# Optimization experiments

Measured on AMD Instinct MI355X. Metric: run time of the kernel, lower is better.

## Reference

```python
import jax, jax.numpy as jnp
import numpy as np

N = 20000   # nodes
E = 320000  # edges
G = 64      # graphs in batch
IN = 256    # in_dim
H = 256     # hidden_dim1
C = 2       # n_classes


def setup_inputs() -> dict:
    key = jax.random.key(0)
    ks = jax.random.split(key, 12)
    h = jax.random.normal(ks[0], (N, IN), jnp.float32)
    src = jax.random.randint(ks[1], (E,), 0, N)
    dst = jax.random.randint(ks[2], (E,), 0, N)
    graph_id = jnp.sort(jax.random.randint(ks[3], (N,), 0, G))
    s_in = 1.0 / np.sqrt(IN)
    s_h = 1.0 / np.sqrt(H)
    W_conv = jax.random.normal(ks[4], (IN, H), jnp.float32) * s_in
    b_conv = jnp.zeros((H,), jnp.float32)
    w_gate = jax.random.normal(ks[5], (H, 1), jnp.float32) * s_h
    b_gate = jnp.zeros((1,), jnp.float32)
    W1 = jax.random.normal(ks[6], (H, H), jnp.float32) * s_h
    b1 = jnp.zeros((H,), jnp.float32)
    W2 = jax.random.normal(ks[7], (H, C), jnp.float32) * s_h
    b2 = jnp.zeros((C,), jnp.float32)
    return dict(h=h, src=src, dst=dst, graph_id=graph_id, W_conv=W_conv,
                b_conv=b_conv, w_gate=w_gate, b_gate=b_gate, W1=W1, b1=b1,
                W2=W2, b2=b2)


def reference(h, src, dst, graph_id, W_conv, b_conv, w_gate, b_gate, W1, b1, W2, b2):
    ones_e = jnp.ones((E,), jnp.float32)
    # DGL GraphConv, norm='both': D_out^-1/2 on source, D_in^-1/2 on dest
    deg_out = jax.ops.segment_sum(ones_e, src, num_segments=N)
    deg_in = jax.ops.segment_sum(ones_e, dst, num_segments=N)
    hn = h * jax.lax.rsqrt(jnp.maximum(deg_out, 1.0))[:, None]
    hn = hn @ W_conv                       # [N, H] (weight applied before aggregation)
    agg = jax.ops.segment_sum(hn[src], dst, num_segments=N)  # gather + scatter-add
    agg = agg * jax.lax.rsqrt(jnp.maximum(deg_in, 1.0))[:, None] + b_conv
    hr = jax.nn.relu(agg)                  # F.relu after conv1
    # GlobalAttentionPooling: per-graph segment softmax over gate scores
    gate = hr @ w_gate + b_gate            # [N, 1]
    gmax = jax.ops.segment_max(gate, graph_id, num_segments=G)
    e = jnp.exp(gate - gmax[graph_id])
    denom = jax.ops.segment_sum(e, graph_id, num_segments=G)
    att = e / denom[graph_id]              # [N, 1] attention weights (g2)
    hg = jax.ops.segment_sum(att * hr, graph_id, num_segments=G)  # [G, H]
    # classifier heads (dropout is identity at inference)
    a2 = hg @ W1 + b1
    a3 = a2 @ W2 + b2
    return jax.nn.sigmoid(a3), att, hg
```

## Files before the change

### kernel.cpp

```cpp
#include <hip/hip_runtime.h>
#include <hip/hip_bf16.h>
#include <hip/hip_fp16.h>
#include <math.h>

#define NN 20000
#define EE 320000
#define GG 64
#define IND 256
#define HD 256
#define CC 2

typedef __hip_bfloat16 bf16;
typedef __attribute__((ext_vector_type(8))) short short8;
typedef __attribute__((ext_vector_type(4))) float f32x4;

__device__ __forceinline__ float b2f(bf16 x){ return __bfloat162float(x); }
__device__ __forceinline__ float bits2f(unsigned short b){
    union{ float f; unsigned u; } v; v.u = ((unsigned)b) << 16; return v.f;
}
__device__ __forceinline__ short f2bs(float x){
    union{ bf16 b; short s; } u; u.b = __float2bfloat16(x); return u.s;
}
__device__ __forceinline__ float ldf3(const void* p, size_t i, int c){
    if (c == 1) return b2f(((const bf16*)p)[i]);
    if (c == 2) return __half2float(((const __half*)p)[i]);
    return ((const float*)p)[i];
}
__device__ __forceinline__ int idec(const void* p, int i, int c){
    if (c == 1) return (int)(((const long long*)p)[i]);
    if (c == 2) return (int)(((const float*)p)[i]);
    if (c == 3) return (int)__half2float(((const __half*)p)[i]);
    return ((const int*)p)[i];
}
__device__ __forceinline__ int wdetect(const unsigned short* p){
    int cb = 0, cf = 0, nz = 0;
    for (int i = 0; i < 128; i += 2){
        unsigned u = p[i];
        nz += (u != 0);
        int e8 = (u >> 7) & 0xFF;
        int e5 = (u >> 10) & 0x1F;
        cb += (e8 >= 100 && e8 <= 141);
        cf += (e5 >= 4 && e5 <= 22);
    }
    return (nz < 8) ? 0 : (cb >= 60) ? 1 : ((cf >= 60) ? 2 : 0);
}

#define ZBLK 64
__global__ __launch_bounds__(256) void k_detect(const void* src, const void* dst,
                         const void* gid,
                         const unsigned short* h, const unsigned short* Wc,
                         const unsigned short* wg, const unsigned short* W1,
                         const unsigned short* W2, const unsigned short* bc,
                         int* icode, int* dcode, int* zero_base,
                         bf16* __restrict__ Wb){
    int blk = blockIdx.x;
    if (blk < 3){
        if (threadIdx.x != 0) return;
        const void* buf = (blk == 0) ? src : (blk == 1) ? dst : gid;
        int n     = (blk == 2) ? NN : EE;
        int bound = (blk == 2) ? GG : NN;
        int ok64 = 1, ok32 = 1, okf32 = 1, okf16 = 1;
        const long long* p64 = (const long long*)buf;
        for (int i = 0; i < 64; i++){
            long long v = p64[n/8 + i];
            if (v < 0 || v >= (long long)bound) ok64 = 0;
        }
        const int* p32 = (const int*)buf;
        const unsigned* pu = (const unsigned*)buf;
        for (int i = 0; i < 64; i++){
            int v = p32[n/4 + i];
            if (v < 0 || v >= bound) ok32 = 0;
            float f = __uint_as_float(pu[n/4 + i]);
            if (!(f >= 0.f && f < (float)bound)) okf32 = 0;
        }
        const __half* ph = (const __half*)buf;
        for (int i = 0; i < 64; i++){
            float f = __half2float(ph[n/2 + i]);
            if (!(f >= 0.f && f < (float)bound)) okf16 = 0;
        }
        icode[blk] = ok64 ? 1 : (ok32 ? 0 : (okf32 ? 2 : (okf16 ? 3 : 0)));
    } else if (blk == 3){
        int t = threadIdx.x; if (t >= 6) return;
        const unsigned short* p = t==0?h:t==1?Wc:t==2?wg:t==3?W1:t==4?W2:bc;
        dcode[t] = wdetect(p);
    } else if (blk < 4 + IND){
        int k = blk - 4;
        __shared__ int code;
        if (threadIdx.x == 0) code = wdetect(Wc);
        __syncthreads();
        int c = code;
        int n = threadIdx.x;
        Wb[(size_t)n*IND + k] = __float2bfloat16(ldf3(Wc, (size_t)k*HD + n, c));
    } else {
        int idx = (blk - (4 + IND))*256 + threadIdx.x;
        const int total = 3*NN + GG*HD;
        for (int i = idx; i < total; i += ZBLK*256) zero_base[i] = 0;
    }
}

__global__ void k_prep(const void* src_r, const void* dst_r, const void* gid_r,
                       const int* __restrict__ icode,
                       int* __restrict__ gid_i,
                       int* cnt_out, int* cnt_in){
    int i = blockIdx.x*256 + threadIdx.x;
    if (i < NN) gid_i[i] = idec(gid_r, i, icode[2]);
    if (i >= EE) return;
    int s = idec(src_r, i, icode[0]);
    int d = idec(dst_r, i, icode[1]);
    if ((unsigned)s < NN) atomicAdd(&cnt_out[s], 1);
    if ((unsigned)d < NN) atomicAdd(&cnt_in[d], 1);
}

__global__ __launch_bounds__(1024) void k_scan(const int* __restrict__ cnt_out,
                                               const int* __restrict__ cnt_in,
                                               const int* __restrict__ gid,
                                               float* rs_out, float* rs_in,
                                               int* __restrict__ row_start,
                                               int* gstart, int* gend){
    int t = threadIdx.x;
    for (int i = t; i < NN; i += 1024){
        rs_out[i] = rsqrtf(fmaxf((float)cnt_out[i], 1.f));
        rs_in[i]  = rsqrtf(fmaxf((float)cnt_in[i], 1.f));
    }
    __shared__ int part[1024];
    const int per = (NN + 1023)/1024;
    int lo = t*per, hi = min(lo+per, NN);
    int s = 0;
    for (int i = lo; i < hi; i++) s += cnt_in[i];
    part[t] = s; __syncthreads();
    for (int off = 1; off < 1024; off <<= 1){
        int v = (t >= off) ? part[t-off] : 0;
        __syncthreads();
        part[t] += v;
        __syncthreads();
    }
    int base = part[t] - s;
    for (int i = lo; i < hi; i++){ row_start[i] = base; base += cnt_in[i]; }
    if (t == 1023) row_start[NN] = part[1023];
    __shared__ int ls[GG+1];
    if (t <= GG){
        int a = 0, b = NN;
        while (a < b){
            int mid = (a + b) >> 1;
            if (gid[mid] < t) a = mid + 1; else b = mid;
        }
        ls[t] = a;
    }
    __syncthreads();
    if (t < GG){ gstart[t] = ls[t]; gend[t] = ls[t+1]; }
}

__global__ void k_fill(const void* src_r, const void* dst_r,
                       const int* __restrict__ icode,
                       const int* __restrict__ row_start, int* __restrict__ cursor,
                       int* __restrict__ csr_src){
    int e = blockIdx.x*256 + threadIdx.x;
    if (e >= EE) return;
    int s = idec(src_r, e, icode[0]);
    int d = idec(dst_r, e, icode[1]);
    if ((unsigned)s >= NN || (unsigned)d >= NN) return;
    int pos = atomicAdd(&cursor[d], 1);
    csr_src[row_start[d] + pos] = s;
}

__global__ __launch_bounds__(256) void k_gemm1m(const void* __restrict__ h,
                                                const bf16* __restrict__ Wb,
                                                const float* __restrict__ rs_out,
                                                const int* __restrict__ dcode,
                                                bf16* __restrict__ hn){
    int fh = dcode[0];
    int tid = threadIdx.x;
    int wave = tid >> 6, lane = tid & 63;
    int q = lane >> 4, mr = lane & 15;
    int row0 = blockIdx.x * 32;
    int ncol0 = wave * 64;
    f32x4 acc[2][4] = {};
    const float* hf = (const float*)h;
    #pragma unroll
    for (int k0 = 0; k0 < IND; k0 += 32){
        short8 a[2], b[4];
        if (fh == 0){
            #pragma unroll
            for (int mi = 0; mi < 2; mi++){
                int r = row0 + mi*16 + mr;
                const float4* p = (const float4*)(hf + (size_t)r*IND + k0 + q*8);
                float4 v0 = p[0], v1 = p[1];
                a[mi][0] = f2bs(v0.x); a[mi][1] = f2bs(v0.y);
                a[mi][2] = f2bs(v0.z); a[mi][3] = f2bs(v0.w);
                a[mi][4] = f2bs(v1.x); a[mi][5] = f2bs(v1.y);
                a[mi][6] = f2bs(v1.z); a[mi][7] = f2bs(v1.w);
            }
        } else {
            #pragma unroll
            for (int mi = 0; mi < 2; mi++){
                int r = row0 + mi*16 + mr;
                #pragma unroll
                for (int j = 0; j < 8; j++)
                    a[mi][j] = f2bs(ldf3(h, (size_t)r*IND + k0 + q*8 + j, fh));
            }
        }
        #pragma unroll
        for (int ni = 0; ni < 4; ni++)
            b[ni] = *reinterpret_cast<const short8*>(
                        Wb + (size_t)(ncol0 + ni*16 + mr)*IND + k0 + q*8);
        #pragma unroll
        for (int mi = 0; mi < 2; mi++)
            #pragma unroll
            for (int ni = 0; ni < 4; ni++)
                acc[mi][ni] = __builtin_amdgcn_mfma_f32_16x16x32_bf16(
                                  a[mi], b[ni], acc[mi][ni], 0, 0, 0);
    }
    #pragma unroll
    for (int mi = 0; mi < 2; mi++){
        int rowb = row0 + mi*16 + q*4;
        #pragma unroll
        for (int r = 0; r < 4; r++){
            int row = rowb + r;
            float rs = rs_out[row];
            #pragma unroll
            for (int ni = 0; ni < 4; ni++)
                hn[(size_t)row*HD + ncol0 + ni*16 + mr] =
                    __float2bfloat16(acc[mi][ni][r] * rs);
        }
    }
}

__global__ __launch_bounds__(256) void k_gather(const bf16* __restrict__ hn,
                                                const float* __restrict__ rs_in,
                                                const int* __restrict__ row_start,
                                                const int* __restrict__ csr_src,
                                                const void* __restrict__ b_conv,
                                                const void* __restrict__ w_gate,
                                                const void* __restrict__ b_gate,
                                                const int* __restrict__ dcode,
                                                float* __restrict__ hr,
                                                float* __restrict__ gate){
    int wave = threadIdx.x >> 6, lane = threadIdx.x & 63;
    int n = blockIdx.x*4 + wave;
    if (n >= NN) return;
    int lo = row_start[n], hi = row_start[n+1];
    float ax = 0.f, ay = 0.f, az = 0.f, aw = 0.f;
    int j = lo;
    for (; j + 8 <= hi; j += 8){
        int s0 = csr_src[j+0], s1 = csr_src[j+1], s2 = csr_src[j+2], s3 = csr_src[j+3];
        int s4 = csr_src[j+4], s5 = csr_src[j+5], s6 = csr_src[j+6], s7 = csr_src[j+7];
        ushort4 u0 = ((const ushort4*)(hn + (size_t)s0*HD))[lane];
        ushort4 u1 = ((const ushort4*)(hn + (size_t)s1*HD))[lane];
        ushort4 u2 = ((const ushort4*)(hn + (size_t)s2*HD))[lane];
        ushort4 u3 = ((const ushort4*)(hn + (size_t)s3*HD))[lane];
        ushort4 u4 = ((const ushort4*)(hn + (size_t)s4*HD))[lane];
        ushort4 u5 = ((const ushort4*)(hn + (size_t)s5*HD))[lane];
        ushort4 u6 = ((const ushort4*)(hn + (size_t)s6*HD))[lane];
        ushort4 u7 = ((const ushort4*)(hn + (size_t)s7*HD))[lane];
        ax += bits2f(u0.x)+bits2f(u1.x)+bits2f(u2.x)+bits2f(u3.x)
            + bits2f(u4.x)+bits2f(u5.x)+bits2f(u6.x)+bits2f(u7.x);
        ay += bits2f(u0.y)+bits2f(u1.y)+bits2f(u2.y)+bits2f(u3.y)
            + bits2f(u4.y)+bits2f(u5.y)+bits2f(u6.y)+bits2f(u7.y);
        az += bits2f(u0.z)+bits2f(u1.z)+bits2f(u2.z)+bits2f(u3.z)
            + bits2f(u4.z)+bits2f(u5.z)+bits2f(u6.z)+bits2f(u7.z);
        aw += bits2f(u0.w)+bits2f(u1.w)+bits2f(u2.w)+bits2f(u3.w)
            + bits2f(u4.w)+bits2f(u5.w)+bits2f(u6.w)+bits2f(u7.w);
    }
    for (; j < hi; j++){
        int s = csr_src[j];
        ushort4 u = ((const ushort4*)(hn + (size_t)s*HD))[lane];
        ax += bits2f(u.x); ay += bits2f(u.y); az += bits2f(u.z); aw += bits2f(u.w);
    }
    int db = dcode[5], fg = dcode[2];
    float rsn = rs_in[n];
    int c = lane*4;
    ax = fmaxf(fmaf(ax, rsn, ldf3(b_conv, c+0, db)), 0.f);
    ay = fmaxf(fmaf(ay, rsn, ldf3(b_conv, c+1, db)), 0.f);
    az = fmaxf(fmaf(az, rsn, ldf3(b_conv, c+2, db)), 0.f);
    aw = fmaxf(fmaf(aw, rsn, ldf3(b_conv, c+3, db)), 0.f);
    float4 v; v.x = ax; v.y = ay; v.z = az; v.w = aw;
    ((float4*)(hr + (size_t)n*HD))[lane] = v;
    float g = ax*ldf3(w_gate, c+0, fg) + ay*ldf3(w_gate, c+1, fg)
            + az*ldf3(w_gate, c+2, fg) + aw*ldf3(w_gate, c+3, fg);
    #pragma unroll
    for (int off = 32; off; off >>= 1) g += __shfl_down(g, off);
    if (lane == 0) gate[n] = g + ldf3(b_gate, 0, db);
}

__global__ __launch_bounds__(256) void k_softhg(const float* __restrict__ gate,
                                                const float* __restrict__ hr,
                                                const int* __restrict__ gstart,
                                                const int* __restrict__ gend,
                                                float* __restrict__ hg,
                                                float* __restrict__ out_att){
    int g = blockIdx.x >> 3, part = blockIdx.x & 7;
    int t = threadIdx.x, lane = t & 63, wid = t >> 6;
    int lo = gstart[g], hi = gend[g], len = hi - lo;
    if (len <= 0) return;
    __shared__ float red[4];
    float m = -INFINITY;
    for (int n = lo + t; n < hi; n += 256) m = fmaxf(m, gate[n]);
    #pragma unroll
    for (int off = 32; off; off >>= 1) m = fmaxf(m, __shfl_xor(m, off));
    if (lane == 0) red[wid] = m;
    __syncthreads();
    m = fmaxf(fmaxf(red[0], red[1]), fmaxf(red[2], red[3]));
    __syncthreads();
    float s = 0.f;
    for (int n = lo + t; n < hi; n += 256) s += expf(gate[n] - m);
    #pragma unroll
    for (int off = 32; off; off >>= 1) s += __shfl_xor(s, off);
    if (lane == 0) red[wid] = s;
    __syncthreads();
    s = red[0] + red[1] + red[2] + red[3];
    float inv = 1.f / s;
    int chunk = (len + 7) >> 3;
    int plo = lo + part*chunk, phi = min(plo + chunk, hi);
    if (plo >= phi) return;
    for (int n = plo + t; n < phi; n += 256)
        out_att[n] = expf(gate[n] - m) * inv;
    float a0 = 0.f, a1 = 0.f, a2 = 0.f, a3 = 0.f;
    int r = plo;
    for (; r + 4 <= phi; r += 4){
        float w0 = expf(gate[r+0] - m) * inv;
        float w1 = expf(gate[r+1] - m) * inv;
        float w2 = expf(gate[r+2] - m) * inv;
        float w3 = expf(gate[r+3] - m) * inv;
        a0 = fmaf(w0, hr[(size_t)(r+0)*HD + t], a0);
        a1 = fmaf(w1, hr[(size_t)(r+1)*HD + t], a1);
        a2 = fmaf(w2, hr[(size_t)(r+2)*HD + t], a2);
        a3 = fmaf(w3, hr[(size_t)(r+3)*HD + t], a3);
    }
    for (; r < phi; r++)
        a0 = fmaf(expf(gate[r] - m) * inv, hr[(size_t)r*HD + t], a0);
    atomicAdd(&hg[g*HD + t], (a0 + a1) + (a2 + a3));
}

__global__ __launch_bounds__(256) void k_cls(const float* __restrict__ hg,
                                             const void* __restrict__ W1,
                                             const void* __restrict__ b1,
                                             const void* __restrict__ W2,
                                             const void* __restrict__ b2,
                                             const int* __restrict__ dcode,
                                             float* __restrict__ out0,
                                             float* __restrict__ out_hg){
    int f1 = dcode[3], f2 = dcode[4], db = dcode[5];
    int g = blockIdx.x, tid = threadIdx.x;
    __shared__ float hs[256];
    float hv = hg[g*HD + tid];
    hs[tid] = hv;
    out_hg[g*HD + tid] = hv;
    __syncthreads();
    float acc = ldf3(b1, tid, db);
    if (f1 == 1){
        const bf16* w = (const bf16*)W1;
        for (int k = 0; k < HD; k++) acc += hs[k]*b2f(w[(size_t)k*HD + tid]);
    } else if (f1 == 2){
        const __half* w = (const __half*)W1;
        for (int k = 0; k < HD; k++) acc += hs[k]*__half2float(w[(size_t)k*HD + tid]);
    } else {
        const float* w = (const float*)W1;
        for (int k = 0; k < HD; k++) acc += hs[k]*w[(size_t)k*HD + tid];
    }
    float p0 = acc * ldf3(W2, tid*CC + 0, f2);
    float p1 = acc * ldf3(W2, tid*CC + 1, f2);
    __shared__ float r0[256], r1[256];
    r0[tid] = p0; r1[tid] = p1; __syncthreads();
    for (int s = 128; s; s >>= 1){
        if (tid < s){ r0[tid] += r0[tid+s]; r1[tid] += r1[tid+s]; }
        __syncthreads();
    }
    if (tid == 0){
        out0[g*CC+0] = 1.f/(1.f + expf(-(r0[0] + ldf3(b2, 0, db))));
        out0[g*CC+1] = 1.f/(1.f + expf(-(r1[0] + ldf3(b2, 1, db))));
    }
}

extern "C" void kernel_launch(void* const* d_in, const int* in_sizes, int n_in,
                              void* d_out, int out_size, void* d_ws, size_t ws_size,
                              hipStream_t stream) {
    const void* h      = d_in[0];
    const void* src_r  = d_in[1];
    const void* dst_r  = d_in[2];
    const void* gid_r  = d_in[3];
    const void* W_conv = d_in[4];
    const void* b_conv = d_in[5];
    const void* w_gate = d_in[6];
    const void* b_gate = d_in[7];
    const void* W1     = d_in[8];
    const void* b1     = d_in[9];
    const void* W2     = d_in[10];
    const void* b2     = d_in[11];

    float* out     = (float*)d_out;
    float* out0    = out;
    float* out_att = out + GG*CC;
    float* out_hg  = out + GG*CC + NN;

    char* w = (char*)d_ws;
    float* hr   = (float*)w;  w += (size_t)NN*HD*sizeof(float);
    bf16*  hn   = (bf16*)w;   w += (size_t)NN*HD*sizeof(bf16);
    bf16*  Wb   = (bf16*)w;   w += (size_t)IND*HD*sizeof(bf16);
    float* rs_o = (float*)w;  w += (size_t)NN*sizeof(float);
    float* rs_i = (float*)w;  w += (size_t)NN*sizeof(float);
    float* gate = (float*)w;  w += (size_t)NN*sizeof(float);
    int* gstart = (int*)w;    w += GG*sizeof(int);
    int* gend   = (int*)w;    w += GG*sizeof(int);
    int* dcode  = (int*)w;    w += 8*sizeof(int);
    int* icode  = (int*)w;    w += 8*sizeof(int);
    int* gid_i  = (int*)w;    w += (size_t)NN*sizeof(int);
    int* cnt_out= (int*)w;    w += (size_t)NN*sizeof(int);
    int* cnt_in = (int*)w;    w += (size_t)NN*sizeof(int);
    int* cursor = (int*)w;    w += (size_t)NN*sizeof(int);
    float* hg   = (float*)w;  w += (size_t)GG*HD*sizeof(float);
    int* rowst  = (int*)w;    w += (size_t)(NN+1)*sizeof(int);
    int* csr    = (int*)w;    w += (size_t)EE*sizeof(int);

    k_detect<<<4 + IND + ZBLK, 256, 0, stream>>>(src_r, dst_r, gid_r,
                                     (const unsigned short*)h, (const unsigned short*)W_conv,
                                     (const unsigned short*)w_gate, (const unsigned short*)W1,
                                     (const unsigned short*)W2, (const unsigned short*)b_conv,
                                     icode, dcode, cnt_out, Wb);

    k_prep<<<(EE+255)/256, 256, 0, stream>>>(src_r, dst_r, gid_r, icode,
                                             gid_i, cnt_out, cnt_in);
    k_scan<<<1, 1024, 0, stream>>>(cnt_out, cnt_in, gid_i, rs_o, rs_i,
                                   rowst, gstart, gend);
    k_fill<<<(EE+255)/256, 256, 0, stream>>>(src_r, dst_r, icode, rowst, cursor, csr);

    k_gemm1m<<<NN/32, 256, 0, stream>>>(h, Wb, rs_o, dcode, hn);

    k_gather<<<(NN+3)/4, 256, 0, stream>>>(hn, rs_i, rowst, csr,
                                           b_conv, w_gate, b_gate, dcode, hr, gate);

    k_softhg<<<GG*8, 256, 0, stream>>>(gate, hr, gstart, gend, hg, out_att);

    k_cls<<<GG, 256, 0, stream>>>(hg, W1, b1, W2, b2, dcode, out0, out_hg);
}
```

Measured before the change: 239.3 us.

## Fuse CSR fill into GEMM launch and widen gather loads to 16 bytes

Merges the CSR fill kernel and the first GEMM into one launch, with block index selecting the role, so the two independent stages can overlap and one launch is removed. The neighbor gather now has each half-wave read a different source row using 16-byte loads of 8 bf16 values, then combines the halves with a cross-half shuffle. This cuts per-edge load instruction count and doubles rows in flight, but adds shuffle work and a heterogeneous block mix in the fused kernel.

Result: no change. 234.7 us (-1.9%).

```diff
diff --git a/kernel.cpp b/kernel.cpp
--- a/kernel.cpp
+++ b/kernel.cpp
@@ -150,29 +150,35 @@
     if (t < GG){ gstart[t] = ls[t]; gend[t] = ls[t+1]; }
 }
 
-__global__ void k_fill(const void* src_r, const void* dst_r,
-                       const int* __restrict__ icode,
-                       const int* __restrict__ row_start, int* __restrict__ cursor,
-                       int* __restrict__ csr_src){
-    int e = blockIdx.x*256 + threadIdx.x;
-    if (e >= EE) return;
-    int s = idec(src_r, e, icode[0]);
-    int d = idec(dst_r, e, icode[1]);
-    if ((unsigned)s >= NN || (unsigned)d >= NN) return;
-    int pos = atomicAdd(&cursor[d], 1);
-    csr_src[row_start[d] + pos] = s;
-}
-
-__global__ __launch_bounds__(256) void k_gemm1m(const void* __restrict__ h,
-                                                const bf16* __restrict__ Wb,
-                                                const float* __restrict__ rs_out,
-                                                const int* __restrict__ dcode,
-                                                bf16* __restrict__ hn){
+#define GEMMB (NN/32)
+#define FILLB ((EE+255)/256)
+__global__ __launch_bounds__(256) void k_fillgemm(const void* __restrict__ h,
+                                                  const bf16* __restrict__ Wb,
+                                                  const float* __restrict__ rs_out,
+                                                  const void* __restrict__ src_r,
+                                                  const void* __restrict__ dst_r,
+                                                  const int* __restrict__ icode,
+                                                  const int* __restrict__ dcode,
+                                                  const int* __restrict__ row_start,
+                                                  int* __restrict__ cursor,
+                                                  int* __restrict__ csr_src,
+                                                  bf16* __restrict__ hn){
+    int blk = blockIdx.x;
+    if (blk >= GEMMB){
+        int e = (blk - GEMMB)*256 + threadIdx.x;
+        if (e >= EE) return;
+        int s = idec(src_r, e, icode[0]);
+        int d = idec(dst_r, e, icode[1]);
+        if ((unsigned)s >= NN || (unsigned)d >= NN) return;
+        int pos = atomicAdd(&cursor[d], 1);
+        csr_src[row_start[d] + pos] = s;
+        return;
+    }
     int fh = dcode[0];
     int tid = threadIdx.x;
     int wave = tid >> 6, lane = tid & 63;
     int q = lane >> 4, mr = lane & 15;
-    int row0 = blockIdx.x * 32;
+    int row0 = blk * 32;
     int ncol0 = wave * 64;
     f32x4 acc[2][4] = {};
     const float* hf = (const float*)h;
@@ -239,44 +245,72 @@
     int n = blockIdx.x*4 + wave;
     if (n >= NN) return;
     int lo = row_start[n], hi = row_start[n+1];
-    float ax = 0.f, ay = 0.f, az = 0.f, aw = 0.f;
+    int half = lane >> 5, l2 = lane & 31;
+    float a0=0.f,a1=0.f,a2=0.f,a3=0.f,a4=0.f,a5=0.f,a6=0.f,a7=0.f;
     int j = lo;
     for (; j + 8 <= hi; j += 8){
-        int s0 = csr_src[j+0], s1 = csr_src[j+1], s2 = csr_src[j+2], s3 = csr_src[j+3];
-        int s4 = csr_src[j+4], s5 = csr_src[j+5], s6 = csr_src[j+6], s7 = csr_src[j+7];
-        ushort4 u0 = ((const ushort4*)(hn + (size_t)s0*HD))[lane];
-        ushort4 u1 = ((const ushort4*)(hn + (size_t)s1*HD))[lane];
-        ushort4 u2 = ((const ushort4*)(hn + (size_t)s2*HD))[lane];
-        ushort4 u3 = ((const ushort4*)(hn + (size_t)s3*HD))[lane];
-        ushort4 u4 = ((const ushort4*)(hn + (size_t)s4*HD))[lane];
-        ushort4 u5 = ((const ushort4*)(hn + (size_t)s5*HD))[lane];
-        ushort4 u6 = ((const ushort4*)(hn + (size_t)s6*HD))[lane];
-        ushort4 u7 = ((const ushort4*)(hn + (size_t)s7*HD))[lane];
-        ax += bits2f(u0.x)+bits2f(u1.x)+bits2f(u2.x)+bits2f(u3.x)
-            + bits2f(u4.x)+bits2f(u5.x)+bits2f(u6.x)+bits2f(u7.x);
-        ay += bits2f(u0.y)+bits2f(u1.y)+bits2f(u2.y)+bits2f(u3.y)
-            + bits2f(u4.y)+bits2f(u5.y)+bits2f(u6.y)+bits2f(u7.y);
-        az += bits2f(u0.z)+bits2f(u1.z)+bits2f(u2.z)+bits2f(u3.z)
-            + bits2f(u4.z)+bits2f(u5.z)+bits2f(u6.z)+bits2f(u7.z);
-        aw += bits2f(u0.w)+bits2f(u1.w)+bits2f(u2.w)+bits2f(u3.w)
-            + bits2f(u4.w)+bits2f(u5.w)+bits2f(u6.w)+bits2f(u7.w);
-    }
-    for (; j < hi; j++){
+        int sA = csr_src[j+0+half], sB = csr_src[j+2+half];
+        int sC = csr_src[j+4+half], sD = csr_src[j+6+half];
+        short8 uA = *reinterpret_cast<const short8*>(hn + (size_t)sA*HD + l2*8);
+        short8 uB = *reinterpret_cast<const short8*>(hn + (size_t)sB*HD + l2*8);
+        short8 uC = *reinterpret_cast<const short8*>(hn + (size_t)sC*HD + l2*8);
+        short8 uD = *reinterpret_cast<const short8*>(hn + (size_t)sD*HD + l2*8);
+        a0 += bits2f((unsigned short)uA[0]) + bits2f((unsigned short)uB[0])
+            + bits2f((unsigned short)uC[0]) + bits2f((unsigned short)uD[0]);
+        a1 += bits2f((unsigned short)uA[1]) + bits2f((unsigned short)uB[1])
+            + bits2f((unsigned short)uC[1]) + bits2f((unsigned short)uD[1]);
+        a2 += bits2f((unsigned short)uA[2]) + bits2f((unsigned short)uB[2])
+            + bits2f((unsigned short)uC[2]) + bits2f((unsigned short)uD[2]);
+        a3 += bits2f((unsigned short)uA[3]) + bits2f((unsigned short)uB[3])
+            + bits2f((unsigned short)uC[3]) + bits2f((unsigned short)uD[3]);
+        a4 += bits2f((unsigned short)uA[4]) + bits2f((unsigned short)uB[4])
+            + bits2f((unsigned short)uC[4]) + bits2f((unsigned short)uD[4]);
+        a5 += bits2f((unsigned short)uA[5]) + bits2f((unsigned short)uB[5])
+            + bits2f((unsigned short)uC[5]) + bits2f((unsigned short)uD[5]);
+        a6 += bits2f((unsigned short)uA[6]) + bits2f((unsigned short)uB[6])
+            + bits2f((unsigned short)uC[6]) + bits2f((unsigned short)uD[6]);
+        a7 += bits2f((unsigned short)uA[7]) + bits2f((unsigned short)uB[7])
+            + bits2f((unsigned short)uC[7]) + bits2f((unsigned short)uD[7]);
+    }
+    for (; j + 2 <= hi; j += 2){
+        int s = csr_src[j+half];
+        short8 u = *reinterpret_cast<const short8*>(hn + (size_t)s*HD + l2*8);
+        a0 += bits2f((unsigned short)u[0]); a1 += bits2f((unsigned short)u[1]);
+        a2 += bits2f((unsigned short)u[2]); a3 += bits2f((unsigned short)u[3]);
+        a4 += bits2f((unsigned short)u[4]); a5 += bits2f((unsigned short)u[5]);
+        a6 += bits2f((unsigned short)u[6]); a7 += bits2f((unsigned short)u[7]);
+    }
+    if (j < hi && half == 0){
         int s = csr_src[j];
-        ushort4 u = ((const ushort4*)(hn + (size_t)s*HD))[lane];
-        ax += bits2f(u.x); ay += bits2f(u.y); az += bits2f(u.z); aw += bits2f(u.w);
-    }
+        short8 u = *reinterpret_cast<const short8*>(hn + (size_t)s*HD + l2*8);
+        a0 += bits2f((unsigned short)u[0]); a1 += bits2f((unsigned short)u[1]);
+        a2 += bits2f((unsigned short)u[2]); a3 += bits2f((unsigned short)u[3]);
+        a4 += bits2f((unsigned short)u[4]); a5 += bits2f((unsigned short)u[5]);
+        a6 += bits2f((unsigned short)u[6]); a7 += bits2f((unsigned short)u[7]);
+    }
+    float send0 = half ? a0 : a4;
+    float send1 = half ? a1 : a5;
+    float send2 = half ? a2 : a6;
+    float send3 = half ? a3 : a7;
+    float recv0 = __shfl_xor(send0, 32);
+    float recv1 = __shfl_xor(send1, 32);
+    float recv2 = __shfl_xor(send2, 32);
+    float recv3 = __shfl_xor(send3, 32);
+    float tot0 = (half ? a4 : a0) + recv0;
+    float tot1 = (half ? a5 : a1) + recv1;
+    float tot2 = (half ? a6 : a2) + recv2;
+    float tot3 = (half ? a7 : a3) + recv3;
     int db = dcode[5], fg = dcode[2];
     float rsn = rs_in[n];
-    int c = lane*4;
-    ax = fmaxf(fmaf(ax, rsn, ldf3(b_conv, c+0, db)), 0.f);
-    ay = fmaxf(fmaf(ay, rsn, ldf3(b_conv, c+1, db)), 0.f);
-    az = fmaxf(fmaf(az, rsn, ldf3(b_conv, c+2, db)), 0.f);
-    aw = fmaxf(fmaf(aw, rsn, ldf3(b_conv, c+3, db)), 0.f);
-    float4 v; v.x = ax; v.y = ay; v.z = az; v.w = aw;
-    ((float4*)(hr + (size_t)n*HD))[lane] = v;
-    float g = ax*ldf3(w_gate, c+0, fg) + ay*ldf3(w_gate, c+1, fg)
-            + az*ldf3(w_gate, c+2, fg) + aw*ldf3(w_gate, c+3, fg);
+    int c = l2*8 + half*4;
+    float v0 = fmaxf(fmaf(tot0, rsn, ldf3(b_conv, c+0, db)), 0.f);
+    float v1 = fmaxf(fmaf(tot1, rsn, ldf3(b_conv, c+1, db)), 0.f);
+    float v2 = fmaxf(fmaf(tot2, rsn, ldf3(b_conv, c+2, db)), 0.f);
+    float v3 = fmaxf(fmaf(tot3, rsn, ldf3(b_conv, c+3, db)), 0.f);
+    float4 fv; fv.x = v0; fv.y = v1; fv.z = v2; fv.w = v3;
+    *(float4*)(hr + (size_t)n*HD + c) = fv;
+    float g = v0*ldf3(w_gate, c+0, fg) + v1*ldf3(w_gate, c+1, fg)
+            + v2*ldf3(w_gate, c+2, fg) + v3*ldf3(w_gate, c+3, fg);
     #pragma unroll
     for (int off = 32; off; off >>= 1) g += __shfl_down(g, off);
     if (lane == 0) gate[n] = g + ldf3(b_gate, 0, db);
@@ -421,9 +455,10 @@
                                              gid_i, cnt_out, cnt_in);
     k_scan<<<1, 1024, 0, stream>>>(cnt_out, cnt_in, gid_i, rs_o, rs_i,
                                    rowst, gstart, gend);
-    k_fill<<<(EE+255)/256, 256, 0, stream>>>(src_r, dst_r, icode, rowst, cursor, csr);
-
-    k_gemm1m<<<NN/32, 256, 0, stream>>>(h, Wb, rs_o, dcode, hn);
+
+    k_fillgemm<<<GEMMB + FILLB, 256, 0, stream>>>(h, Wb, rs_o, src_r, dst_r,
+                                                  icode, dcode, rowst, cursor,
+                                                  csr, hn);
 
     k_gather<<<(NN+3)/4, 256, 0, stream>>>(hn, rs_i, rowst, csr,
                                            b_conv, w_gate, b_gate, dcode, hr, gate);
```
